# Optimization experiments

Hardware: AMD Instinct MI355X
Metric: run time of the kernel (lower is better)

The kernel has to match this reference:

```python
import jax, jax.numpy as jnp
import numpy as np

B, S, D = 8, 1024, 768
H, HD = 12, 64
FF = 3072
EPS = 1e-5


def layernorm(x, w, b):
    mu = jnp.mean(x, axis=-1, keepdims=True)
    var = jnp.mean(jnp.square(x - mu), axis=-1, keepdims=True)
    return (x - mu) / jnp.sqrt(var + EPS) * w + b


def setup_inputs() -> dict:
    key = jax.random.key(0)
    ks = jax.random.split(key, 16)
    s_in = 1.0 / np.sqrt(D)
    s_p = 1.0 / np.sqrt(H * HD)
    s_ff = 1.0 / np.sqrt(FF)
    return {
        "x": jax.random.normal(ks[0], (B, S, D), dtype=jnp.float32),
        "ln1_w": jnp.ones((D,), jnp.float32),
        "ln1_b": jnp.zeros((D,), jnp.float32),
        "Wq": jax.random.uniform(ks[1], (H, D, HD), jnp.float32, -s_in, s_in),
        "bq": jax.random.uniform(ks[2], (H, HD), jnp.float32, -s_in, s_in),
        "Wk": jax.random.uniform(ks[3], (H, D, HD), jnp.float32, -s_in, s_in),
        "bk": jax.random.uniform(ks[4], (H, HD), jnp.float32, -s_in, s_in),
        "Wv": jax.random.uniform(ks[5], (H, D, HD), jnp.float32, -s_in, s_in),
        "bv": jax.random.uniform(ks[6], (H, HD), jnp.float32, -s_in, s_in),
        "Wp": jax.random.uniform(ks[7], (H * HD, D), jnp.float32, -s_p, s_p),
        "bp": jax.random.uniform(ks[8], (D,), jnp.float32, -s_p, s_p),
        "ln2_w": jnp.ones((D,), jnp.float32),
        "ln2_b": jnp.zeros((D,), jnp.float32),
        "W1": jax.random.uniform(ks[9], (D, FF), jnp.float32, -s_in, s_in),
        "b1": jax.random.uniform(ks[10], (FF,), jnp.float32, -s_in, s_in),
        "W2": jax.random.uniform(ks[11], (FF, D), jnp.float32, -s_ff, s_ff),
        "b2": jax.random.uniform(ks[12], (D,), jnp.float32, -s_ff, s_ff),
    }


def reference(x, ln1_w, ln1_b, Wq, bq, Wk, bk, Wv, bv, Wp, bp,
              ln2_w, ln2_b, W1, b1, W2, b2):
    gelu = lambda t: jax.nn.gelu(t, approximate=False)
    # --- multi-head self attention (NOTE: original never applies scale) ---
    y = layernorm(x, ln1_w, ln1_b)                       # [B,S,D]
    q = jnp.einsum('bsd,hde->bhse', y, Wq) + bq[:, None, :][None]
    k = jnp.einsum('bsd,hde->bhse', y, Wk) + bk[:, None, :][None]
    v = jnp.einsum('bsd,hde->bhse', y, Wv) + bv[:, None, :][None]
    attn = jax.nn.softmax(jnp.einsum('bhse,bhte->bhst', q, k), axis=-1)
    out = jnp.einsum('bhst,bhte->bhse', attn, v)         # [B,H,S,HD]
    out = out.transpose(0, 2, 1, 3).reshape(x.shape[0], x.shape[1], -1)  # concat heads
    y = gelu(out @ Wp + bp)                              # projection + GELU
    x = x + y                                            # residual 1
    # --- MLP block ---
    h = layernorm(x, ln2_w, ln2_b)
    h = gelu(h @ W1 + b1)
    h = gelu(h @ W2 + b2)
    return x + h                                         # residual 2
```

## Files before the change

### kernel.cpp

```cpp
#include <hip/hip_runtime.h>
#include <hip/hip_bf16.h>
#include <math.h>

#define BB 8
#define SS 1024
#define DD 768
#define HH 12
#define HDD 64
#define FFF 3072
#define NROW (BB*SS)
#define QKVN (3*DD)

typedef __hip_bfloat16 bf16;
typedef __bf16 bf16x8 __attribute__((ext_vector_type(8)));
typedef float floatx4 __attribute__((ext_vector_type(4)));

__device__ __forceinline__ float gelu_fast(float x) {
    float u = x * fmaf(0.07135481627f, x * x, 1.595769122f);
    float e = __expf(u);
    return x * e * __builtin_amdgcn_rcpf(e + 1.0f);
}

__device__ __forceinline__ unsigned short f2bfbits(float f) {
    bf16 h = __float2bfloat16(f);
    return __builtin_bit_cast(unsigned short, h);
}

__device__ __forceinline__ void gload16(const void* g, void* l) {
    __builtin_amdgcn_global_load_lds(
        (const __attribute__((address_space(1))) unsigned int*)g,
        (__attribute__((address_space(3))) unsigned int*)l, 16, 0, 0);
}

template<typename T>
__global__ __launch_bounds__(256) void ln_kernel(const T* __restrict__ x,
                                                 const float* __restrict__ w,
                                                 const float* __restrict__ b,
                                                 bf16* __restrict__ y) {
    int wave = threadIdx.x >> 6, lane = threadIdx.x & 63;
    int row = blockIdx.x * 4 + wave;
    const T* xr = x + (size_t)row * DD;
    bf16* yr = y + (size_t)row * DD;

    float v[12];
    #pragma unroll
    for (int s = 0; s < 3; s++) {
        int base = s * 256 + lane * 4;
        if constexpr (__is_same(T, float)) {
            float4 f = *(const float4*)(xr + base);
            v[s*4+0] = f.x; v[s*4+1] = f.y; v[s*4+2] = f.z; v[s*4+3] = f.w;
        } else {
            ushort4 u = *(const ushort4*)(xr + base);
            v[s*4+0] = __bfloat162float(__builtin_bit_cast(bf16, u.x));
            v[s*4+1] = __bfloat162float(__builtin_bit_cast(bf16, u.y));
            v[s*4+2] = __bfloat162float(__builtin_bit_cast(bf16, u.z));
            v[s*4+3] = __bfloat162float(__builtin_bit_cast(bf16, u.w));
        }
    }
    float sum = 0.f, sq = 0.f;
    #pragma unroll
    for (int i = 0; i < 12; i++) { sum += v[i]; sq += v[i] * v[i]; }
    #pragma unroll
    for (int off = 1; off < 64; off <<= 1) {
        sum += __shfl_xor(sum, off, 64);
        sq  += __shfl_xor(sq,  off, 64);
    }
    float mu  = sum * (1.0f / DD);
    float var = sq * (1.0f / DD) - mu * mu;
    float inv = rsqrtf(var + 1e-5f);

    #pragma unroll
    for (int s = 0; s < 3; s++) {
        int base = s * 256 + lane * 4;
        float4 wf = *(const float4*)(w + base);
        float4 bf = *(const float4*)(b + base);
        ushort4 o;
        o.x = f2bfbits((v[s*4+0] - mu) * inv * wf.x + bf.x);
        o.y = f2bfbits((v[s*4+1] - mu) * inv * wf.y + bf.y);
        o.z = f2bfbits((v[s*4+2] - mu) * inv * wf.z + bf.z);
        o.w = f2bfbits((v[s*4+3] - mu) * inv * wf.w + bf.w);
        *(ushort4*)(yr + base) = o;
    }
}

__global__ __launch_bounds__(256) void prep_kernel(
    const float* __restrict__ Wq, const float* __restrict__ Wk,
    const float* __restrict__ Wv, const float* __restrict__ Wp,
    const float* __restrict__ W1, const float* __restrict__ W2,
    const float* __restrict__ bq, const float* __restrict__ bk,
    const float* __restrict__ bv,
    bf16* __restrict__ Wqkvt, bf16* __restrict__ Wpt,
    bf16* __restrict__ W1t, bf16* __restrict__ W2t, float* __restrict__ bqkv)
{
    int id = blockIdx.x;
    if (id >= 6912) {
        int i = (id - 6912) * 256 + threadIdx.x;
        if (i < DD) { bqkv[i] = bq[i]; bqkv[DD + i] = bk[i]; bqkv[2*DD + i] = bv[i]; }
        return;
    }
    const float* src; bf16* dst; int K, N, hmode, local;
    if (id < 1728)      { K = DD;  N = DD;  hmode = 1; local = id % 576;
                          src = (id < 576) ? Wq : (id < 1152 ? Wk : Wv);
                          dst = Wqkvt + (size_t)(id / 576) * DD * DD; }
    else if (id < 2304) { K = DD;  N = DD;  hmode = 0; local = id - 1728; src = Wp; dst = Wpt; }
    else if (id < 4608) { K = DD;  N = FFF; hmode = 0; local = id - 2304; src = W1; dst = W1t; }
    else                { K = FFF; N = DD;  hmode = 0; local = id - 4608; src = W2; dst = W2t; }
    int ktiles = K / 32;
    int k0 = (local % ktiles) * 32, n0 = (local / ktiles) * 32;
    __shared__ float t[32][33];
    int tx = threadIdx.x & 31, ty4 = threadIdx.x >> 5;
    #pragma unroll
    for (int i = 0; i < 4; i++) {
        int k = k0 + ty4 * 4 + i;
        int n = n0 + tx;
        size_t si = hmode ? ((size_t)(n >> 6) * K * 64 + (size_t)k * 64 + (n & 63))
                          : ((size_t)k * N + n);
        t[ty4 * 4 + i][tx] = src[si];
    }
    __syncthreads();
    #pragma unroll
    for (int i = 0; i < 4; i++) {
        int n = n0 + ty4 * 4 + i;
        int k = k0 + tx;
        dst[(size_t)n * K + k] = __float2bfloat16(t[tx][ty4 * 4 + i]);
    }
}

template<int MT, int KH, int DEPTH>
__global__ __launch_bounds__(256) void mfma_gemm(
    const bf16* __restrict__ A, const bf16* __restrict__ Bt,
    const float* __restrict__ bias, const float* __restrict__ residf,
    const bf16* __restrict__ residb, void* __restrict__ Cout,
    int M, int N, int K, int act, int out_bf16, int nx, int py,
    int qkvmode, bf16* __restrict__ qhg, bf16* __restrict__ khg, bf16* __restrict__ vtg)
{
    constexpr int MFRAG = MT / 32;
    constexpr int ACH = MT * 4;
    constexpr int A_LOADS = ACH * KH / 256;
    constexpr int B_LOADS = 2 * KH;
    constexpr int LOADS = A_LOADS + B_LOADS;
    constexpr unsigned ABYTES = KH * MT * 32 * 2;
    constexpr unsigned BBYTES = KH * 128 * 32 * 2;
    static_assert(DEPTH == 2 || (DEPTH == 3 && LOADS == 4), "vmcnt literal fixed at 4");
    __shared__ bf16 As[DEPTH][KH * MT * 32];
    __shared__ bf16 Bs[DEPTH][KH * 128 * 32];
    int tid = threadIdx.x;
    int id = blockIdx.x;
    int xcd = id & 7, slot = id >> 3;
    int rp = slot % py, ct = slot / py;
    int row0 = (xcd * py + rp) * MT, col0 = ct * 128;
    int wave = tid >> 6, lane = tid & 63;
    int wm = (wave >> 1) * (MT / 2), wn = (wave & 1) * 64;
    int l16 = lane & 15, quad = lane >> 4;

    const bf16* pA[A_LOADS]; unsigned ldA[A_LOADS];
    #pragma unroll
    for (int i = 0; i < A_LOADS; i++) {
        int c = tid + i * 256;
        int half = c / ACH, rem = c % ACH;
        int r = rem >> 2, pos = rem & 3;
        int ksw = half * 32 + ((pos ^ ((r >> 1) & 3)) << 3);
        pA[i] = A + (size_t)(row0 + r) * K + ksw;
        ldA[i] = (unsigned)c * 16u;
    }
    const bf16* pB[B_LOADS]; unsigned ldB[B_LOADS];
    #pragma unroll
    for (int i = 0; i < B_LOADS; i++) {
        int c = tid + i * 256;
        int half = c >> 9, rem = c & 511;
        int r = rem >> 2, pos = rem & 3;
        int ksw = half * 32 + ((pos ^ ((r >> 1) & 3)) << 3);
        pB[i] = Bt + (size_t)(col0 + r) * K + ksw;
        ldB[i] = (unsigned)c * 16u;
    }
    char* lbaseA = (char*)&As[0][0];
    char* lbaseB = (char*)&Bs[0][0];

    auto stage = [&](int k0, int buf) {
        char* dA = lbaseA + (unsigned)buf * ABYTES;
        char* dB = lbaseB + (unsigned)buf * BBYTES;
        #pragma unroll
        for (int i = 0; i < A_LOADS; i++) gload16(pA[i] + k0, dA + ldA[i]);
        #pragma unroll
        for (int i = 0; i < B_LOADS; i++) gload16(pB[i] + k0, dB + ldB[i]);
    };

    unsigned roA[KH][MFRAG], roB[KH][4];
    #pragma unroll
    for (int s = 0; s < KH; s++) {
        #pragma unroll
        for (int mt = 0; mt < MFRAG; mt++) {
            int r = wm + mt * 16 + l16;
            int pos = quad ^ ((r >> 1) & 3);
            roA[s][mt] = (unsigned)(s * MT * 32 + r * 32 + pos * 8) * 2u;
        }
        #pragma unroll
        for (int nt = 0; nt < 4; nt++) {
            int r = wn + nt * 16 + l16;
            int pos = quad ^ ((r >> 1) & 3);
            roB[s][nt] = (unsigned)(s * 4096 + r * 32 + pos * 8) * 2u;
        }
    }

    floatx4 acc[MFRAG][4] = {};

    auto compute = [&](int cur) {
        const char* bA = lbaseA + (unsigned)cur * ABYTES;
        const char* bB = lbaseB + (unsigned)cur * BBYTES;
        #pragma unroll
        for (int s = 0; s < KH; s++) {
            bf16x8 af[MFRAG], bfr[4];
            #pragma unroll
            for (int mt = 0; mt < MFRAG; mt++)
                af[mt] = *(const bf16x8*)(bA + roA[s][mt]);
            #pragma unroll
            for (int nt = 0; nt < 4; nt++)
                bfr[nt] = *(const bf16x8*)(bB + roB[s][nt]);
            #pragma unroll
            for (int mt = 0; mt < MFRAG; mt++)
                #pragma unroll
                for (int nt = 0; nt < 4; nt++)
                    acc[mt][nt] = __builtin_amdgcn_mfma_f32_16x16x32_bf16(
                        af[mt], bfr[nt], acc[mt][nt], 0, 0, 0);
        }
    };

    if constexpr (DEPTH == 3) {
        int T = K / (32 * KH);
        stage(0, 0);
        if (T > 1) stage(32 * KH, 1);
        for (int t = 0; t < T; t++) {
            if (t == T - 1) { asm volatile("s_waitcnt vmcnt(0)" ::: "memory"); }
            else            { asm volatile("s_waitcnt vmcnt(4)" ::: "memory"); }
            __builtin_amdgcn_s_barrier();
            if (t + 2 < T) stage((t + 2) * (32 * KH), (t + 2) % 3);
            compute(t % 3);
        }
    } else {
        stage(0, 0);
        int cur = 0;
        for (int k0 = 0; k0 < K; k0 += 32 * KH) {
            __syncthreads();
            if (k0 + 32 * KH < K) stage(k0 + 32 * KH, cur ^ 1);
            compute(cur);
            cur ^= 1;
        }
    }

    if (qkvmode) {
        #pragma unroll
        for (int mt = 0; mt < MFRAG; mt++) {
            int rbase = row0 + wm + mt * 16 + quad * 4;
            int bq_ = rbase >> 10, sb = rbase & 1023;
            #pragma unroll
            for (int nt = 0; nt < 4; nt++) {
                int col = col0 + wn + nt * 16 + l16;
                float bcol = bias[col];
                if (col < DD) {
                    int hh = col >> 6, e = col & 63;
                    bf16* base = qhg + (((size_t)bq_ * HH + hh) * SS + sb) * 64 + e;
                    #pragma unroll
                    for (int r = 0; r < 4; r++)
                        base[(size_t)r * 64] = __float2bfloat16(acc[mt][nt][r] + bcol);
                } else if (col < 2 * DD) {
                    int cc = col - DD, hh = cc >> 6, e = cc & 63;
                    bf16* base = khg + (((size_t)bq_ * HH + hh) * SS) * 64;
                    #pragma unroll
                    for (int r = 0; r < 4; r++) {
                        int s = sb + r;
                        int pos = (((e >> 3) ^ (s & 7)) << 3) | (e & 7);
                        base[(size_t)s * 64 + pos] = __float2bfloat16(acc[mt][nt][r] + bcol);
                    }
                } else {
                    int cc = col - 2 * DD, hh = cc >> 6, e = cc & 63;
                    int c_t = sb >> 3;
                    int sc = (c_t & ~7) | ((c_t & 7) ^ (e & 7));
                    size_t off = (((size_t)bq_ * HH + hh) * 64 + e) * SS + sc * 8 + (sb & 7);
                    ushort4 pk;
                    pk.x = f2bfbits(acc[mt][nt][0] + bcol);
                    pk.y = f2bfbits(acc[mt][nt][1] + bcol);
                    pk.z = f2bfbits(acc[mt][nt][2] + bcol);
                    pk.w = f2bfbits(acc[mt][nt][3] + bcol);
                    *(ushort4*)&vtg[off] = pk;
                }
            }
        }
        return;
    }

    #pragma unroll
    for (int mt = 0; mt < MFRAG; mt++) {
        int rbase = row0 + wm + mt * 16 + quad * 4;
        #pragma unroll
        for (int nt = 0; nt < 4; nt++) {
            int col = col0 + wn + nt * 16 + l16;
            float bcol = bias[col];
            #pragma unroll
            for (int r = 0; r < 4; r++) {
                int row = rbase + r;
                float v = acc[mt][nt][r] + bcol;
                if (act) v = gelu_fast(v);
                if (residf) v += residf[(size_t)row * N + col];
                if (residb) v += __bfloat162float(residb[(size_t)row * N + col]);
                if (out_bf16) ((bf16*)Cout)[(size_t)row * N + col] = __float2bfloat16(v);
                else          ((float*)Cout)[(size_t)row * N + col] = v;
            }
        }
    }
}

__global__ __launch_bounds__(256) void attn_mfma(
    const bf16* __restrict__ qh, const bf16* __restrict__ kh,
    const bf16* __restrict__ vT, bf16* __restrict__ ao)
{
    __shared__ bf16 Ks[2][64 * 64];
    __shared__ bf16 Vs[2][64 * 64];
    __shared__ bf16 Ps[128 * 64];

    int tid = threadIdx.x;
    int wave = tid >> 6, lane = tid & 63;
    int l16 = lane & 15, quad = lane >> 4;
    int id = blockIdx.x;
    int bh = (id & 7) * 12 + ((id >> 3) >> 3);
    int b = bh / HH, h = bh % HH;
    int s0 = ((id >> 3) & 7) * 128;
    int wm = wave * 32;

    const bf16* qbase = qh + ((size_t)bh * SS) * HDD;
    const bf16* kbase = kh + ((size_t)bh * SS) * HDD;
    const bf16* vbase = vT + ((size_t)bh * HDD) * SS;

    auto stage = [&](int t0, int buf) {
        #pragma unroll
        for (int i = 0; i < 2; i++) {
            int c = tid + i * 256;
            gload16(kbase + (size_t)t0 * 64 + c * 8, &Ks[buf][c * 8]);
            gload16(vbase + (size_t)(c >> 3) * SS + t0 + (c & 7) * 8, &Vs[buf][c * 8]);
        }
    };

    bf16x8 qf[2][2];
    #pragma unroll
    for (int mt = 0; mt < 2; mt++)
        #pragma unroll
        for (int ks = 0; ks < 2; ks++)
            qf[mt][ks] = *(const bf16x8*)(qbase +
                (size_t)(s0 + wm + mt * 16 + l16) * HDD + ks * 32 + quad * 8);

    floatx4 oaccT[4][2] = {};
    float lsum[2] = {};

    stage(0, 0);
    int cur = 0;
    for (int t0 = 0; t0 < SS; t0 += 64) {
        __syncthreads();
        if (t0 + 64 < SS) stage(t0 + 64, cur ^ 1);

        floatx4 st[4][2] = {};
        #pragma unroll
        for (int tt = 0; tt < 4; tt++) {
            int t = tt * 16 + l16;
            #pragma unroll
            for (int ks = 0; ks < 2; ks++) {
                int pos = (quad + 4 * ks) ^ (t & 7);
                bf16x8 kf = *(const bf16x8*)(&Ks[cur][t * 64 + pos * 8]);
                #pragma unroll
                for (int mt = 0; mt < 2; mt++)
                    st[tt][mt] = __builtin_amdgcn_mfma_f32_16x16x32_bf16(
                        kf, qf[mt][ks], st[tt][mt], 0, 0, 0);
            }
        }

        #pragma unroll
        for (int tt = 0; tt < 4; tt++)
            #pragma unroll
            for (int mt = 0; mt < 2; mt++) {
                float p0 = __expf(st[tt][mt][0]);
                float p1 = __expf(st[tt][mt][1]);
                float p2 = __expf(st[tt][mt][2]);
                float p3 = __expf(st[tt][mt][3]);
                lsum[mt] += (p0 + p1) + (p2 + p3);
                int m = wm + mt * 16 + l16;
                int c = tt * 2 + (quad >> 1);
                ushort4 pk;
                pk.x = f2bfbits(p0); pk.y = f2bfbits(p1);
                pk.z = f2bfbits(p2); pk.w = f2bfbits(p3);
                *(ushort4*)&Ps[m * 64 + ((c ^ (m & 7)) << 3) + (quad & 1) * 4] = pk;
            }

        #pragma unroll
        for (int ks = 0; ks < 2; ks++) {
            bf16x8 pf[2];
            #pragma unroll
            for (int mt = 0; mt < 2; mt++) {
                int m = wm + mt * 16 + l16;
                pf[mt] = *(const bf16x8*)(&Ps[m * 64 + (((quad + 4 * ks) ^ (m & 7)) << 3)]);
            }
            #pragma unroll
            for (int et = 0; et < 4; et++) {
                int e = et * 16 + l16;
                int vpos = (quad + 4 * ks) ^ (e & 7);
                bf16x8 vf = *(const bf16x8*)(&Vs[cur][e * 64 + vpos * 8]);
                #pragma unroll
                for (int mt = 0; mt < 2; mt++)
                    oaccT[et][mt] = __builtin_amdgcn_mfma_f32_16x16x32_bf16(
                        vf, pf[mt], oaccT[et][mt], 0, 0, 0);
            }
        }
        cur ^= 1;
    }

    float linv[2];
    #pragma unroll
    for (int mt = 0; mt < 2; mt++) {
        float l = lsum[mt];
        l += __shfl_xor(l, 16, 64);
        l += __shfl_xor(l, 32, 64);
        linv[mt] = __builtin_amdgcn_rcpf(l);
    }
    #pragma unroll
    for (int et = 0; et < 4; et++)
        #pragma unroll
        for (int mt = 0; mt < 2; mt++) {
            int m = wm + mt * 16 + l16;
            int c = et * 2 + (quad >> 1);
            ushort4 pk;
            pk.x = f2bfbits(oaccT[et][mt][0] * linv[mt]);
            pk.y = f2bfbits(oaccT[et][mt][1] * linv[mt]);
            pk.z = f2bfbits(oaccT[et][mt][2] * linv[mt]);
            pk.w = f2bfbits(oaccT[et][mt][3] * linv[mt]);
            *(ushort4*)&Ps[m * 64 + ((c ^ (m & 7)) << 3) + (quad & 1) * 4] = pk;
        }
    int mrow = wm + (lane >> 1);
    bf16* op = ao + ((size_t)b * SS + s0 + mrow) * DD + h * HDD;
    #pragma unroll
    for (int i = 0; i < 4; i++) {
        int j = (lane & 1) * 4 + i;
        bf16x8 v = *(const bf16x8*)&Ps[mrow * 64 + ((j ^ (mrow & 7)) << 3)];
        *(bf16x8*)&op[j * 8] = v;
    }
}

extern "C" void kernel_launch(void* const* d_in, const int* in_sizes, int n_in,
                              void* d_out, int out_size, void* d_ws, size_t ws_size,
                              hipStream_t stream)
{
    (void)in_sizes; (void)n_in; (void)out_size; (void)ws_size;
    const float* x    = (const float*)d_in[0];
    const float* ln1w = (const float*)d_in[1];
    const float* ln1b = (const float*)d_in[2];
    const float* Wq   = (const float*)d_in[3];
    const float* bq   = (const float*)d_in[4];
    const float* Wk   = (const float*)d_in[5];
    const float* bk   = (const float*)d_in[6];
    const float* Wv   = (const float*)d_in[7];
    const float* bv   = (const float*)d_in[8];
    const float* Wp   = (const float*)d_in[9];
    const float* bp   = (const float*)d_in[10];
    const float* ln2w = (const float*)d_in[11];
    const float* ln2b = (const float*)d_in[12];
    const float* W1   = (const float*)d_in[13];
    const float* b1   = (const float*)d_in[14];
    const float* W2   = (const float*)d_in[15];
    const float* b2   = (const float*)d_in[16];
    float* out = (float*)d_out;

    char* p = (char*)d_ws;
    auto alloc = [&](size_t bytes) { char* r = p; p += (bytes + 255) & ~255ull; return r; };
    bf16*  Wqkvt = (bf16*)alloc((size_t)QKVN * DD * 2);
    bf16*  Wpt   = (bf16*)alloc((size_t)DD * DD * 2);
    bf16*  W1t   = (bf16*)alloc((size_t)FFF * DD * 2);
    bf16*  W2t   = (bf16*)alloc((size_t)DD * FFF * 2);
    float* bqkv  = (float*)alloc((size_t)QKVN * 4);
    bf16*  yb    = (bf16*)alloc((size_t)NROW * DD * 2);
    bf16*  x1b   = (bf16*)alloc((size_t)NROW * DD * 2);
    char*  dynr  = alloc((size_t)NROW * DD * 2 + 3 * ((size_t)NROW * DD * 2));
    bf16*  aob   = (bf16*)dynr;
    bf16*  qhb   = (bf16*)(dynr + (size_t)NROW * DD * 2);
    bf16*  khb   = qhb + (size_t)NROW * DD;
    bf16*  vtb   = khb + (size_t)NROW * DD;
    bf16*  hb    = (bf16*)dynr;

    prep_kernel<<<6915, 256, 0, stream>>>(Wq, Wk, Wv, Wp, W1, W2, bq, bk, bv,
                                          Wqkvt, Wpt, W1t, W2t, bqkv);

    ln_kernel<float><<<NROW/4, 256, 0, stream>>>(x, ln1w, ln1b, yb);

    mfma_gemm<128,1,3><<<1152, 256, 0, stream>>>(
        yb, Wqkvt, bqkv, nullptr, nullptr, nullptr, NROW, QKVN, DD, 0, 0, 18, 8,
        1, qhb, khb, vtb);

    attn_mfma<<<dim3(BB*HH*(SS/128)), 256, 0, stream>>>(qhb, khb, vtb, aob);

    mfma_gemm<64,2,2><<<768, 256, 0, stream>>>(
        aob, Wpt, bp, x, nullptr, x1b, NROW, DD, DD, 1, 1, 6, 16,
        0, nullptr, nullptr, nullptr);

    ln_kernel<bf16><<<NROW/4, 256, 0, stream>>>(x1b, ln2w, ln2b, yb);

    mfma_gemm<64,2,2><<<3072, 256, 0, stream>>>(
        yb, W1t, b1, nullptr, nullptr, hb, NROW, FFF, DD, 1, 1, 24, 16,
        0, nullptr, nullptr, nullptr);

    mfma_gemm<64,2,2><<<768, 256, 0, stream>>>(
        hb, W2t, b2, nullptr, x1b, out, NROW, DD, FFF, 1, 0, 6, 16,
        0, nullptr, nullptr, nullptr);
}
```

Before: 364.5 us.

## Add 256x128-tile 512-thread MFMA GEMM for the MLP matmuls

Introduces a new GEMM kernel with 256x128 block tiles, 8 waves, swizzled LDS layout, double-buffered async global-to-LDS loads split into two K-halves, and raised wave priority around the MFMA blocks. It replaces the smaller-tile GEMM for the W1 and W2 MLP matmuls, aiming at more data reuse per block and better overlap of loads with MFMA work. The W2 GEMM launches only 192 blocks, which may underfill the GPU, and the larger LDS footprint limits occupancy.

```diff
diff --git a/kernel.cpp b/kernel.cpp
--- a/kernel.cpp
+++ b/kernel.cpp
@@ -309,6 +309,113 @@
     }
 }
 
+__global__ __launch_bounds__(512) void gemm8(
+    const bf16* __restrict__ A, const bf16* __restrict__ Bt,
+    const float* __restrict__ bias, const bf16* __restrict__ residb,
+    void* __restrict__ Cout, int N, int K, int act, int out_bf16, int py)
+{
+    __shared__ bf16 As[2][2][256 * 32];
+    __shared__ bf16 Bs[2][2][128 * 32];
+    int tid = threadIdx.x;
+    int id = blockIdx.x;
+    int xcd = id & 7, slot = id >> 3;
+    int rp = slot % py, ct = slot / py;
+    int row0 = (xcd * py + rp) * 256, col0 = ct * 128;
+    int wave = tid >> 6, lane = tid & 63;
+    int wm = (wave >> 1) * 64, wn = (wave & 1) * 64;
+    int l16 = lane & 15, quad = lane >> 4;
+
+    const bf16* pA[2]; unsigned ldA[2];
+    #pragma unroll
+    for (int i = 0; i < 2; i++) {
+        int c = tid + i * 512;
+        int r = c >> 2, pos = c & 3;
+        pA[i] = A + (size_t)(row0 + r) * K + ((pos ^ ((r >> 1) & 3)) << 3);
+        ldA[i] = (unsigned)c * 16u;
+    }
+    const bf16* pB; unsigned ldB;
+    {
+        int r = tid >> 2, pos = tid & 3;
+        pB = Bt + (size_t)(col0 + r) * K + ((pos ^ ((r >> 1) & 3)) << 3);
+        ldB = (unsigned)tid * 16u;
+    }
+    auto stage = [&](int kt, int buf, int s) {
+        int kof = kt * 64 + s * 32;
+        char* dA = (char*)&As[buf][s][0];
+        char* dB = (char*)&Bs[buf][s][0];
+        gload16(pA[0] + kof, dA + ldA[0]);
+        gload16(pA[1] + kof, dA + ldA[1]);
+        gload16(pB + kof, dB + ldB);
+    };
+
+    unsigned roA[4], roB[4];
+    #pragma unroll
+    for (int mt = 0; mt < 4; mt++) {
+        int r = wm + mt * 16 + l16;
+        int pos = quad ^ ((r >> 1) & 3);
+        roA[mt] = (unsigned)(r * 32 + pos * 8) * 2u;
+    }
+    #pragma unroll
+    for (int nt = 0; nt < 4; nt++) {
+        int r = wn + nt * 16 + l16;
+        int pos = quad ^ ((r >> 1) & 3);
+        roB[nt] = (unsigned)(r * 32 + pos * 8) * 2u;
+    }
+
+    floatx4 acc[4][4] = {};
+    int KT = K >> 6;
+
+    stage(0, 0, 0);
+    stage(0, 0, 1);
+
+    for (int t = 0; t < KT; t++) {
+        int cb = t & 1;
+        #pragma unroll
+        for (int s = 0; s < 2; s++) {
+            if (s == 1 && t == KT - 1) { asm volatile("s_waitcnt vmcnt(0)" ::: "memory"); }
+            else                       { asm volatile("s_waitcnt vmcnt(3)" ::: "memory"); }
+            __builtin_amdgcn_s_barrier();
+            const char* bA = (const char*)&As[cb][s][0];
+            const char* bB = (const char*)&Bs[cb][s][0];
+            bf16x8 af[4], bfr[4];
+            #pragma unroll
+            for (int mt = 0; mt < 4; mt++) af[mt] = *(const bf16x8*)(bA + roA[mt]);
+            #pragma unroll
+            for (int nt = 0; nt < 4; nt++) bfr[nt] = *(const bf16x8*)(bB + roB[nt]);
+            if (t + 1 < KT) stage(t + 1, cb ^ 1, s);
+            asm volatile("s_waitcnt lgkmcnt(0)" ::: "memory");
+            __builtin_amdgcn_sched_barrier(0);
+            __builtin_amdgcn_s_setprio(1);
+            #pragma unroll
+            for (int mt = 0; mt < 4; mt++)
+                #pragma unroll
+                for (int nt = 0; nt < 4; nt++)
+                    acc[mt][nt] = __builtin_amdgcn_mfma_f32_16x16x32_bf16(
+                        af[mt], bfr[nt], acc[mt][nt], 0, 0, 0);
+            __builtin_amdgcn_s_setprio(0);
+        }
+    }
+
+    #pragma unroll
+    for (int mt = 0; mt < 4; mt++) {
+        int rbase = row0 + wm + mt * 16 + quad * 4;
+        #pragma unroll
+        for (int nt = 0; nt < 4; nt++) {
+            int col = col0 + wn + nt * 16 + l16;
+            float bcol = bias[col];
+            #pragma unroll
+            for (int r = 0; r < 4; r++) {
+                int row = rbase + r;
+                float v = acc[mt][nt][r] + bcol;
+                if (act) v = gelu_fast(v);
+                if (residb) v += __bfloat162float(residb[(size_t)row * N + col]);
+                if (out_bf16) ((bf16*)Cout)[(size_t)row * N + col] = __float2bfloat16(v);
+                else          ((float*)Cout)[(size_t)row * N + col] = v;
+            }
+        }
+    }
+}
+
 __global__ __launch_bounds__(256) void attn_mfma(
     const bf16* __restrict__ qh, const bf16* __restrict__ kh,
     const bf16* __restrict__ vT, bf16* __restrict__ ao)
@@ -498,11 +605,7 @@
 
     ln_kernel<bf16><<<NROW/4, 256, 0, stream>>>(x1b, ln2w, ln2b, yb);
 
-    mfma_gemm<64,2,2><<<3072, 256, 0, stream>>>(
-        yb, W1t, b1, nullptr, nullptr, hb, NROW, FFF, DD, 1, 1, 24, 16,
-        0, nullptr, nullptr, nullptr);
-
-    mfma_gemm<64,2,2><<<768, 256, 0, stream>>>(
-        hb, W2t, b2, nullptr, x1b, out, NROW, DD, FFF, 1, 0, 6, 16,
-        0, nullptr, nullptr, nullptr);
-}
+    gemm8<<<768, 512, 0, stream>>>(yb, W1t, b1, nullptr, hb, FFF, DD, 1, 1, 4);
+
+    gemm8<<<192, 512, 0, stream>>>(hb, W2t, b2, x1b, out, DD, FFF, 1, 0, 4);
+}
```

Result: slower. 380.8 us (+4.5%).

## Fuse LN1 into weight prep launch and shrink attention blocks to 64 queries

Applied to the files above, without the earlier changes.

The first layernorm is folded into the weight-transpose prep kernel as extra blocks, which removes one kernel launch and lets the two independent pieces of work overlap. The attention kernel now uses 128-thread blocks covering 64 query rows instead of 256 threads covering 128. That doubles the grid and halves the P shared buffer, aiming for more resident blocks and better load balance. In exchange, each K/V tile is reloaded by twice as many blocks, and each thread issues more staging loads.

```diff
diff --git a/kernel.cpp b/kernel.cpp
--- a/kernel.cpp
+++ b/kernel.cpp
@@ -33,15 +33,10 @@
 }
 
 template<typename T>
-__global__ __launch_bounds__(256) void ln_kernel(const T* __restrict__ x,
-                                                 const float* __restrict__ w,
-                                                 const float* __restrict__ b,
-                                                 bf16* __restrict__ y) {
-    int wave = threadIdx.x >> 6, lane = threadIdx.x & 63;
-    int row = blockIdx.x * 4 + wave;
-    const T* xr = x + (size_t)row * DD;
-    bf16* yr = y + (size_t)row * DD;
-
+__device__ __forceinline__ void ln_row(const T* __restrict__ xr,
+                                       const float* __restrict__ w,
+                                       const float* __restrict__ b,
+                                       bf16* __restrict__ yr, int lane) {
     float v[12];
     #pragma unroll
     for (int s = 0; s < 3; s++) {
@@ -68,7 +63,6 @@
     float mu  = sum * (1.0f / DD);
     float var = sq * (1.0f / DD) - mu * mu;
     float inv = rsqrtf(var + 1e-5f);
-
     #pragma unroll
     for (int s = 0; s < 3; s++) {
         int base = s * 256 + lane * 4;
@@ -83,16 +77,34 @@
     }
 }
 
-__global__ __launch_bounds__(256) void prep_kernel(
+template<typename T>
+__global__ __launch_bounds__(256) void ln_kernel(const T* __restrict__ x,
+                                                 const float* __restrict__ w,
+                                                 const float* __restrict__ b,
+                                                 bf16* __restrict__ y) {
+    int wave = threadIdx.x >> 6, lane = threadIdx.x & 63;
+    int row = blockIdx.x * 4 + wave;
+    ln_row<T>(x + (size_t)row * DD, w, b, y + (size_t)row * DD, lane);
+}
+
+__global__ __launch_bounds__(256) void setup_kernel(
     const float* __restrict__ Wq, const float* __restrict__ Wk,
     const float* __restrict__ Wv, const float* __restrict__ Wp,
     const float* __restrict__ W1, const float* __restrict__ W2,
     const float* __restrict__ bq, const float* __restrict__ bk,
     const float* __restrict__ bv,
     bf16* __restrict__ Wqkvt, bf16* __restrict__ Wpt,
-    bf16* __restrict__ W1t, bf16* __restrict__ W2t, float* __restrict__ bqkv)
+    bf16* __restrict__ W1t, bf16* __restrict__ W2t, float* __restrict__ bqkv,
+    const float* __restrict__ x, const float* __restrict__ ln1w,
+    const float* __restrict__ ln1b, bf16* __restrict__ yb)
 {
     int id = blockIdx.x;
+    if (id >= 6915) {
+        int wave = threadIdx.x >> 6, lane = threadIdx.x & 63;
+        int row = (id - 6915) * 4 + wave;
+        ln_row<float>(x + (size_t)row * DD, ln1w, ln1b, yb + (size_t)row * DD, lane);
+        return;
+    }
     if (id >= 6912) {
         int i = (id - 6912) * 256 + threadIdx.x;
         if (i < DD) { bqkv[i] = bq[i]; bqkv[DD + i] = bk[i]; bqkv[2*DD + i] = bv[i]; }
@@ -309,21 +321,22 @@
     }
 }
 
-__global__ __launch_bounds__(256) void attn_mfma(
+__global__ __launch_bounds__(128) void attn_mfma(
     const bf16* __restrict__ qh, const bf16* __restrict__ kh,
     const bf16* __restrict__ vT, bf16* __restrict__ ao)
 {
     __shared__ bf16 Ks[2][64 * 64];
     __shared__ bf16 Vs[2][64 * 64];
-    __shared__ bf16 Ps[128 * 64];
+    __shared__ bf16 Ps[64 * 64];
 
     int tid = threadIdx.x;
     int wave = tid >> 6, lane = tid & 63;
     int l16 = lane & 15, quad = lane >> 4;
     int id = blockIdx.x;
-    int bh = (id & 7) * 12 + ((id >> 3) >> 3);
+    int slot = id >> 3;
+    int bh = (id & 7) * 12 + (slot >> 4);
     int b = bh / HH, h = bh % HH;
-    int s0 = ((id >> 3) & 7) * 128;
+    int s0 = (slot & 15) * 64;
     int wm = wave * 32;
 
     const bf16* qbase = qh + ((size_t)bh * SS) * HDD;
@@ -332,8 +345,8 @@
 
     auto stage = [&](int t0, int buf) {
         #pragma unroll
-        for (int i = 0; i < 2; i++) {
-            int c = tid + i * 256;
+        for (int i = 0; i < 4; i++) {
+            int c = tid + i * 128;
             gload16(kbase + (size_t)t0 * 64 + c * 8, &Ks[buf][c * 8]);
             gload16(vbase + (size_t)(c >> 3) * SS + t0 + (c & 7) * 8, &Vs[buf][c * 8]);
         }
@@ -481,16 +494,15 @@
     bf16*  vtb   = khb + (size_t)NROW * DD;
     bf16*  hb    = (bf16*)dynr;
 
-    prep_kernel<<<6915, 256, 0, stream>>>(Wq, Wk, Wv, Wp, W1, W2, bq, bk, bv,
-                                          Wqkvt, Wpt, W1t, W2t, bqkv);
-
-    ln_kernel<float><<<NROW/4, 256, 0, stream>>>(x, ln1w, ln1b, yb);
+    setup_kernel<<<8963, 256, 0, stream>>>(Wq, Wk, Wv, Wp, W1, W2, bq, bk, bv,
+                                           Wqkvt, Wpt, W1t, W2t, bqkv,
+                                           x, ln1w, ln1b, yb);
 
     mfma_gemm<128,1,3><<<1152, 256, 0, stream>>>(
         yb, Wqkvt, bqkv, nullptr, nullptr, nullptr, NROW, QKVN, DD, 0, 0, 18, 8,
         1, qhb, khb, vtb);
 
-    attn_mfma<<<dim3(BB*HH*(SS/128)), 256, 0, stream>>>(qhb, khb, vtb, aob);
+    attn_mfma<<<dim3(BB*HH*(SS/64)), 128, 0, stream>>>(qhb, khb, vtb, aob);
 
     mfma_gemm<64,2,2><<<768, 256, 0, stream>>>(
         aob, Wpt, bp, x, nullptr, x1b, NROW, DD, DD, 1, 1, 6, 16,
```

New measurement: 375.4 us. 3.0% more time.
